# Kernel optimization log

Hardware: AMD Instinct MI355X
Metric: run time of the kernel (lower is better)

The kernel has to match this reference:

```python
import jax, jax.numpy as jnp
import numpy as np

ALPHA = 0.2

def _ema_last_weights(T, alpha, dtype):
    # Closed form for the final EMA value after the sequential recurrence:
    # ema_T = (1-a)^(T-1) * x_0 + sum_{t=1}^{T-1} a*(1-a)^(T-1-t) * x_t
    t = jnp.arange(T)
    w = alpha * (1.0 - alpha) ** (T - 1 - t)
    w = w.at[0].set((1.0 - alpha) ** (T - 1))
    return w.astype(dtype)


def setup_inputs() -> dict:
    key = jax.random.key(0)
    k1, k2 = jax.random.split(key)
    B, T, F = 64, 2048, 256
    x = jax.random.normal(k1, (B, T, F), dtype=jnp.float32)
    W = jax.random.normal(k2, (F, F), dtype=jnp.float32) * (1.0 / np.sqrt(F))
    b = jnp.zeros((F,), dtype=jnp.float32)
    return {"x": x, "W": W, "b": b}


def reference(x, W, b):
    B, T, F = x.shape
    # final-step EMA over time (equivalent to the sequential python loop)
    w = _ema_last_weights(T, ALPHA, x.dtype)          # [T]
    last_ref = jnp.einsum('t,btf->bf', w, x)[:, None, :]  # [B,1,F]
    # base residual predictor: per-timestep linear
    res = jnp.einsum('btf,fg->btg', x, W) + b          # [B,T,F]
    return last_ref + res
```

## Files before the change

### kernel.cpp

```cpp
#include <hip/hip_runtime.h>

#define Bdim 64
#define Tdim 2048
#define Fdim 256
#define TAIL 256
#define NCH 8
#define CHT 32

#define BK 32
#define NCHUNK 8
#define PFD 2

typedef __bf16 bf16x8 __attribute__((ext_vector_type(8)));
typedef float f32x16 __attribute__((ext_vector_type(16)));
typedef unsigned short u16x8 __attribute__((ext_vector_type(8)));

__device__ __forceinline__ unsigned short bf16_rne(float f) {
  unsigned int u = __float_as_uint(f);
  u += 0x7FFFu + ((u >> 16) & 1u);
  return (unsigned short)(u >> 16);
}

__global__ void prep(const float* __restrict__ x, const float* __restrict__ W,
                     unsigned short* __restrict__ Wf, float* __restrict__ part) {
  int blk = blockIdx.x;
  if (blk < Fdim) {
    int o = blk * 256 + threadIdx.x;
    int e = o & 7, lane = (o >> 3) & 63, nsub = (o >> 9) & 7, s = (o >> 12) & 1;
    int c = o >> 13;
    int n = nsub * 32 + (lane & 31);
    int k = c * 32 + (2 * s + (lane >> 5)) * 8 + e;
    Wf[o] = bf16_rne(W[k * Fdim + n]);
  } else {
    int j = blk - Fdim;
    int b = j & 63, c = j >> 6;
    int f = threadIdx.x;
    int t0 = Tdim - TAIL + c * CHT;
    float w = 0.2f * exp2f((float)(Tdim - 1 - t0) * -0.32192809488736235f);
    const float* xp = x + ((size_t)b * Tdim + t0) * Fdim + f;
    float s = 0.f;
#pragma unroll
    for (int q = 0; q < CHT; ++q) {
      s += w * xp[(size_t)q * Fdim];
      w *= 1.25f;
    }
    part[(c * Bdim + b) * Fdim + f] = s;
  }
}

__global__ __launch_bounds__(256, 3)
void gemm_fused(const float* __restrict__ x, const unsigned short* __restrict__ Wf,
                const float* __restrict__ bias, const float* __restrict__ part,
                float* __restrict__ out) {
  __shared__ float lref[Fdim];

  const int tid = threadIdx.x;
  const int blk = blockIdx.x;
  const int b = blk >> 5;
  const size_t row0 = (size_t)blk * 64;

  const int wave = tid >> 6;
  const int mw = wave >> 1;
  const int nw = wave & 1;
  const int lane = tid & 63;
  const int lm = lane & 31;
  const int half = lane >> 5;

  {
    float s = bias[tid];
#pragma unroll
    for (int c = 0; c < NCH; ++c) s += part[(c * Bdim + b) * Fdim + tid];
    lref[tid] = s;
  }
  __syncthreads();

  const float* ax = x + (row0 + mw * 32 + lm) * Fdim;
  const unsigned short* bx = Wf + (size_t)(nw * 4) * 512 + lane * 8;

  f32x16 acc[4] = {};
  float4 Ar[PFD][2][2];
  bf16x8 Bf[2][4];

#pragma unroll
  for (int p = 0; p < PFD; ++p) {
#pragma unroll
    for (int s = 0; s < 2; ++s) {
      const float* sp = ax + p * BK + (2 * s + half) * 8;
      Ar[p][s][0] = *(const float4*)sp;
      Ar[p][s][1] = *(const float4*)(sp + 4);
    }
  }
#pragma unroll
  for (int s = 0; s < 2; ++s)
#pragma unroll
    for (int j = 0; j < 4; ++j)
      Bf[s][j] = *(const bf16x8*)(bx + (size_t)(s * 8 + j) * 512);

#pragma unroll
  for (int c = 0; c < NCHUNK; ++c) {
    const int slot = c % PFD;
#pragma unroll
    for (int s = 0; s < 2; ++s) {
      float4 v0 = Ar[slot][s][0], v1 = Ar[slot][s][1];
      u16x8 w;
      w[0] = bf16_rne(v0.x); w[1] = bf16_rne(v0.y);
      w[2] = bf16_rne(v0.z); w[3] = bf16_rne(v0.w);
      w[4] = bf16_rne(v1.x); w[5] = bf16_rne(v1.y);
      w[6] = bf16_rne(v1.z); w[7] = bf16_rne(v1.w);
      bf16x8 af;
      *(u16x8*)&af = w;
      acc[0] = __builtin_amdgcn_mfma_f32_32x32x16_bf16(af, Bf[s][0], acc[0], 0, 0, 0);
      acc[1] = __builtin_amdgcn_mfma_f32_32x32x16_bf16(af, Bf[s][1], acc[1], 0, 0, 0);
      acc[2] = __builtin_amdgcn_mfma_f32_32x32x16_bf16(af, Bf[s][2], acc[2], 0, 0, 0);
      acc[3] = __builtin_amdgcn_mfma_f32_32x32x16_bf16(af, Bf[s][3], acc[3], 0, 0, 0);
      if (c + 1 < NCHUNK) {
#pragma unroll
        for (int j = 0; j < 4; ++j)
          Bf[s][j] = *(const bf16x8*)(bx + (size_t)(((c + 1) * 2 + s) * 8 + j) * 512);
      }
    }
    if (c + PFD < NCHUNK) {
#pragma unroll
      for (int s = 0; s < 2; ++s) {
        const float* sp = ax + (c + PFD) * BK + (2 * s + half) * 8;
        Ar[slot][s][0] = *(const float4*)sp;
        Ar[slot][s][1] = *(const float4*)(sp + 4);
      }
    }
  }

  float* op = out + (row0 + mw * 32) * Fdim + nw * 128;
  const int rbase = 4 * half;
#pragma unroll
  for (int j = 0; j < 4; ++j) {
    float lb = lref[nw * 128 + j * 32 + lm];
#pragma unroll
    for (int r = 0; r < 16; ++r) {
      int rowi = (r & 3) + 8 * (r >> 2) + rbase;
      op[(size_t)rowi * Fdim + j * 32 + lm] = acc[j][r] + lb;
    }
  }
}

extern "C" void kernel_launch(void* const* d_in, const int* in_sizes, int n_in,
                              void* d_out, int out_size, void* d_ws, size_t ws_size,
                              hipStream_t stream) {
  const float* x = (const float*)d_in[0];
  const float* W = (const float*)d_in[1];
  const float* bias = (const float*)d_in[2];
  float* out = (float*)d_out;

  unsigned short* Wf = (unsigned short*)d_ws;
  float* part = (float*)((char*)d_ws + Fdim * Fdim * sizeof(unsigned short));

  prep<<<Fdim + Bdim * NCH, 256, 0, stream>>>(x, W, Wf, part);
  gemm_fused<<<(Bdim * Tdim) / 64, 256, 0, stream>>>(x, Wf, bias, part, out);
}
```

Baseline: 285.7 us.

## Stage bf16 A fragments in LDS and retile waves to 64x64 output tiles

Before, each wave loaded and converted its own 32-row A slice straight from global memory, so two waves redundantly converted the same rows. Now all threads cooperatively load the 64x256 fp32 A tile once, convert it to bf16, and write it into a padded, XOR-swizzled LDS fragment layout. Each wave then computes a 64x64 output tile (2x2 MFMA blocks) with A fragments read from LDS, and the W fragment layout is reordered to match. The trade-offs are about 33KB of LDS per block, which may reduce occupancy, and an up-front sync, since global loads of A are no longer overlapped with the MFMAs.

```diff
diff --git a/kernel.cpp b/kernel.cpp
--- a/kernel.cpp
+++ b/kernel.cpp
@@ -7,9 +7,8 @@
 #define NCH 8
 #define CHT 32
 
-#define BK 32
 #define NCHUNK 8
-#define PFD 2
+#define FR_STR 520
 
 typedef __bf16 bf16x8 __attribute__((ext_vector_type(8)));
 typedef float f32x16 __attribute__((ext_vector_type(16)));
@@ -26,9 +25,9 @@
   int blk = blockIdx.x;
   if (blk < Fdim) {
     int o = blk * 256 + threadIdx.x;
-    int e = o & 7, lane = (o >> 3) & 63, nsub = (o >> 9) & 7, s = (o >> 12) & 1;
-    int c = o >> 13;
-    int n = nsub * 32 + (lane & 31);
+    int e = o & 7, lane = (o >> 3) & 63, wh = (o >> 9) & 1, s = (o >> 10) & 1;
+    int c = (o >> 11) & 7, w = o >> 14;
+    int n = w * 64 + wh * 32 + (lane & 31);
     int k = c * 32 + (2 * s + (lane >> 5)) * 8 + e;
     Wf[o] = bf16_rne(W[k * Fdim + n]);
   } else {
@@ -52,6 +51,7 @@
 void gemm_fused(const float* __restrict__ x, const unsigned short* __restrict__ Wf,
                 const float* __restrict__ bias, const float* __restrict__ part,
                 float* __restrict__ out) {
+  __shared__ unsigned short Afrag[32 * FR_STR];
   __shared__ float lref[Fdim];
 
   const int tid = threadIdx.x;
@@ -60,11 +60,23 @@
   const size_t row0 = (size_t)blk * 64;
 
   const int wave = tid >> 6;
-  const int mw = wave >> 1;
-  const int nw = wave & 1;
   const int lane = tid & 63;
   const int lm = lane & 31;
   const int half = lane >> 5;
+
+  const int r = tid >> 2, q = tid & 3;
+  const int iw = r >> 5;
+  const int sq = q >> 1, hb = q & 1;
+  const int dl = hb * 32 + (r & 31);
+  const int wpos = dl ^ ((dl >> 5) << 2);
+  const float* ap = x + (row0 + r) * Fdim + q * 8;
+
+  float4 av[8][2];
+#pragma unroll
+  for (int p = 0; p < 8; ++p) {
+    av[p][0] = *(const float4*)(ap + p * 32);
+    av[p][1] = *(const float4*)(ap + p * 32 + 4);
+  }
 
   {
     float s = bias[tid];
@@ -72,72 +84,70 @@
     for (int c = 0; c < NCH; ++c) s += part[(c * Bdim + b) * Fdim + tid];
     lref[tid] = s;
   }
+
+#pragma unroll
+  for (int p = 0; p < 8; ++p) {
+    float4 v0 = av[p][0], v1 = av[p][1];
+    u16x8 w;
+    w[0] = bf16_rne(v0.x); w[1] = bf16_rne(v0.y);
+    w[2] = bf16_rne(v0.z); w[3] = bf16_rne(v0.w);
+    w[4] = bf16_rne(v1.x); w[5] = bf16_rne(v1.y);
+    w[6] = bf16_rne(v1.z); w[7] = bf16_rne(v1.w);
+    const int fragidx = (p * 2 + iw) * 2 + sq;
+    *(u16x8*)&Afrag[fragidx * FR_STR + wpos * 8] = w;
+  }
   __syncthreads();
 
-  const float* ax = x + (row0 + mw * 32 + lm) * Fdim;
-  const unsigned short* bx = Wf + (size_t)(nw * 4) * 512 + lane * 8;
+  const unsigned short* bx = Wf + (size_t)wave * (32 * 512) + lane * 8;
+  const int rpos = lane ^ ((lane >> 5) << 2);
+  const unsigned short* abase = &Afrag[rpos * 8];
 
-  f32x16 acc[4] = {};
-  float4 Ar[PFD][2][2];
-  bf16x8 Bf[2][4];
+  f32x16 acc[2][2] = {};
+  bf16x8 Bf[2][2][2];
 
 #pragma unroll
-  for (int p = 0; p < PFD; ++p) {
+  for (int cc = 0; cc < 2; ++cc)
 #pragma unroll
-    for (int s = 0; s < 2; ++s) {
-      const float* sp = ax + p * BK + (2 * s + half) * 8;
-      Ar[p][s][0] = *(const float4*)sp;
-      Ar[p][s][1] = *(const float4*)(sp + 4);
-    }
-  }
+    for (int s = 0; s < 2; ++s)
 #pragma unroll
-  for (int s = 0; s < 2; ++s)
-#pragma unroll
-    for (int j = 0; j < 4; ++j)
-      Bf[s][j] = *(const bf16x8*)(bx + (size_t)(s * 8 + j) * 512);
+      for (int wh = 0; wh < 2; ++wh)
+        Bf[cc][s][wh] = *(const bf16x8*)(bx + (size_t)(cc * 4 + s * 2 + wh) * 512);
 
 #pragma unroll
   for (int c = 0; c < NCHUNK; ++c) {
-    const int slot = c % PFD;
+    const int par = c & 1;
 #pragma unroll
     for (int s = 0; s < 2; ++s) {
-      float4 v0 = Ar[slot][s][0], v1 = Ar[slot][s][1];
-      u16x8 w;
-      w[0] = bf16_rne(v0.x); w[1] = bf16_rne(v0.y);
-      w[2] = bf16_rne(v0.z); w[3] = bf16_rne(v0.w);
-      w[4] = bf16_rne(v1.x); w[5] = bf16_rne(v1.y);
-      w[6] = bf16_rne(v1.z); w[7] = bf16_rne(v1.w);
-      bf16x8 af;
-      *(u16x8*)&af = w;
-      acc[0] = __builtin_amdgcn_mfma_f32_32x32x16_bf16(af, Bf[s][0], acc[0], 0, 0, 0);
-      acc[1] = __builtin_amdgcn_mfma_f32_32x32x16_bf16(af, Bf[s][1], acc[1], 0, 0, 0);
-      acc[2] = __builtin_amdgcn_mfma_f32_32x32x16_bf16(af, Bf[s][2], acc[2], 0, 0, 0);
-      acc[3] = __builtin_amdgcn_mfma_f32_32x32x16_bf16(af, Bf[s][3], acc[3], 0, 0, 0);
-      if (c + 1 < NCHUNK) {
+      bf16x8 a0 = *(const bf16x8*)&abase[((c * 2 + 0) * 2 + s) * FR_STR];
+      bf16x8 a1 = *(const bf16x8*)&abase[((c * 2 + 1) * 2 + s) * FR_STR];
+      acc[0][0] = __builtin_amdgcn_mfma_f32_32x32x16_bf16(a0, Bf[par][s][0], acc[0][0], 0, 0, 0);
+      acc[0][1] = __builtin_amdgcn_mfma_f32_32x32x16_bf16(a0, Bf[par][s][1], acc[0][1], 0, 0, 0);
+      acc[1][0] = __builtin_amdgcn_mfma_f32_32x32x16_bf16(a1, Bf[par][s][0], acc[1][0], 0, 0, 0);
+      acc[1][1] = __builtin_amdgcn_mfma_f32_32x32x16_bf16(a1, Bf[par][s][1], acc[1][1], 0, 0, 0);
+    }
+    if (c + 2 < NCHUNK) {
 #pragma unroll
-        for (int j = 0; j < 4; ++j)
-          Bf[s][j] = *(const bf16x8*)(bx + (size_t)(((c + 1) * 2 + s) * 8 + j) * 512);
-      }
-    }
-    if (c + PFD < NCHUNK) {
+      for (int s = 0; s < 2; ++s)
 #pragma unroll
-      for (int s = 0; s < 2; ++s) {
-        const float* sp = ax + (c + PFD) * BK + (2 * s + half) * 8;
-        Ar[slot][s][0] = *(const float4*)sp;
-        Ar[slot][s][1] = *(const float4*)(sp + 4);
-      }
+        for (int wh = 0; wh < 2; ++wh)
+          Bf[par][s][wh] =
+              *(const bf16x8*)(bx + (size_t)((c + 2) * 4 + s * 2 + wh) * 512);
     }
   }
 
-  float* op = out + (row0 + mw * 32) * Fdim + nw * 128;
+  float* op = out + row0 * Fdim;
   const int rbase = 4 * half;
 #pragma unroll
-  for (int j = 0; j < 4; ++j) {
-    float lb = lref[nw * 128 + j * 32 + lm];
+  for (int i = 0; i < 2; ++i) {
 #pragma unroll
-    for (int r = 0; r < 16; ++r) {
-      int rowi = (r & 3) + 8 * (r >> 2) + rbase;
-      op[(size_t)rowi * Fdim + j * 32 + lm] = acc[j][r] + lb;
+    for (int j = 0; j < 2; ++j) {
+      int n = wave * 64 + j * 32 + lm;
+      float lb = lref[n];
+#pragma unroll
+      for (int rr = 0; rr < 16; ++rr) {
+        int rowi = i * 32 + (rr & 3) + 8 * (rr >> 2) + rbase;
+        op[(size_t)rowi * Fdim + n] = acc[i][j][rr] + lb;
+      }
     }
   }
 }
```

Result: faster. 243.1 us (-14.9%).

## Stage A tiles through per-wave LDS for coalesced row loads, reorder W fragments

Applied to the files above, without the earlier changes.

Changes the A-operand loading so each lane reads a 32-float contiguous row segment (eight lanes covering a row's 128-byte span). The values are converted to bf16 and written into a per-wave double-buffered LDS tile, then read back in MFMA fragment layout. The W fragment layout in prep is reordered so each wave's B reads are contiguous. The bias-plus-EMA reference is now kept per thread in registers, which removes the shared array and the __syncthreads. This trades strided global reads for an extra LDS round trip and more LDS usage, which may affect occupancy.

```diff
diff --git a/kernel.cpp b/kernel.cpp
--- a/kernel.cpp
+++ b/kernel.cpp
@@ -7,12 +7,11 @@
 #define NCH 8
 #define CHT 32
 
-#define BK 32
 #define NCHUNK 8
-#define PFD 2
 
 typedef __bf16 bf16x8 __attribute__((ext_vector_type(8)));
 typedef float f32x16 __attribute__((ext_vector_type(16)));
+typedef unsigned short u16x4 __attribute__((ext_vector_type(4)));
 typedef unsigned short u16x8 __attribute__((ext_vector_type(8)));
 
 __device__ __forceinline__ unsigned short bf16_rne(float f) {
@@ -23,18 +22,19 @@
 
 __global__ void prep(const float* __restrict__ x, const float* __restrict__ W,
                      unsigned short* __restrict__ Wf, float* __restrict__ part) {
-  int blk = blockIdx.x;
+  const int blk = blockIdx.x;
+  const int tid = threadIdx.x;
   if (blk < Fdim) {
-    int o = blk * 256 + threadIdx.x;
-    int e = o & 7, lane = (o >> 3) & 63, nsub = (o >> 9) & 7, s = (o >> 12) & 1;
-    int c = o >> 13;
-    int n = nsub * 32 + (lane & 31);
+    int o = blk * 256 + tid;
+    int e = o & 7, lane = (o >> 3) & 63, wh = (o >> 9) & 1, s = (o >> 10) & 1;
+    int c = (o >> 11) & 7, w = o >> 14;
+    int n = w * 64 + wh * 32 + (lane & 31);
     int k = c * 32 + (2 * s + (lane >> 5)) * 8 + e;
     Wf[o] = bf16_rne(W[k * Fdim + n]);
   } else {
     int j = blk - Fdim;
     int b = j & 63, c = j >> 6;
-    int f = threadIdx.x;
+    int f = tid;
     int t0 = Tdim - TAIL + c * CHT;
     float w = 0.2f * exp2f((float)(Tdim - 1 - t0) * -0.32192809488736235f);
     const float* xp = x + ((size_t)b * Tdim + t0) * Fdim + f;
@@ -52,88 +52,103 @@
 void gemm_fused(const float* __restrict__ x, const unsigned short* __restrict__ Wf,
                 const float* __restrict__ bias, const float* __restrict__ part,
                 float* __restrict__ out) {
-  __shared__ float lref[Fdim];
+  __shared__ unsigned short At[4][2][2][520];
 
   const int tid = threadIdx.x;
   const int blk = blockIdx.x;
   const int b = blk >> 5;
-  const size_t row0 = (size_t)blk * 64;
-
   const int wave = tid >> 6;
   const int mw = wave >> 1;
   const int nw = wave & 1;
   const int lane = tid & 63;
   const int lm = lane & 31;
   const int half = lane >> 5;
+  const size_t mt = (size_t)blk * 2 + mw;
 
-  {
-    float s = bias[tid];
+  float lref[4];
 #pragma unroll
-    for (int c = 0; c < NCH; ++c) s += part[(c * Bdim + b) * Fdim + tid];
-    lref[tid] = s;
+  for (int j = 0; j < 4; ++j) {
+    int n = nw * 128 + j * 32 + lm;
+    float s = bias[n];
+#pragma unroll
+    for (int c = 0; c < NCH; ++c) s += part[(c * Bdim + b) * Fdim + n];
+    lref[j] = s;
   }
-  __syncthreads();
 
-  const float* ax = x + (row0 + mw * 32 + lm) * Fdim;
-  const unsigned short* bx = Wf + (size_t)(nw * 4) * 512 + lane * 8;
+  const int arow = lane >> 3;
+  const int acol = (lane & 7) * 4;
+  const float* ax = x + (mt * 32 + arow) * Fdim + acol;
+  const int ds_ = ((lane & 7) >> 2);
+  const int dhb = ((lane & 7) >> 1) & 1;
+  const int dh2 = lane & 1;
+
+  const unsigned short* bx = Wf + lane * 8;
+#define BOFF(c, s, sub) \
+  ((size_t)(((nw * 2 + ((sub) >> 1)) * 32 + (c) * 4 + (s) * 2 + ((sub) & 1))) * 512)
 
   f32x16 acc[4] = {};
-  float4 Ar[PFD][2][2];
+  float4 Ar[2][4];
   bf16x8 Bf[2][4];
 
-#pragma unroll
-  for (int p = 0; p < PFD; ++p) {
-#pragma unroll
-    for (int s = 0; s < 2; ++s) {
-      const float* sp = ax + p * BK + (2 * s + half) * 8;
-      Ar[p][s][0] = *(const float4*)sp;
-      Ar[p][s][1] = *(const float4*)(sp + 4);
-    }
+#define ALOAD(k, slot)                                             \
+  {                                                                \
+    const float* s4 = ax + (k) * 32;                               \
+    Ar[slot][0] = *(const float4*)(s4);                            \
+    Ar[slot][1] = *(const float4*)(s4 + 8 * Fdim);                 \
+    Ar[slot][2] = *(const float4*)(s4 + 16 * Fdim);                \
+    Ar[slot][3] = *(const float4*)(s4 + 24 * Fdim);                \
   }
+#define ACVT(slot, buf)                                            \
+  {                                                                \
+    _Pragma("unroll") for (int p = 0; p < 4; ++p) {                \
+      float4 v = Ar[slot][p];                                      \
+      u16x4 wv;                                                    \
+      wv[0] = bf16_rne(v.x); wv[1] = bf16_rne(v.y);                \
+      wv[2] = bf16_rne(v.z); wv[3] = bf16_rne(v.w);                \
+      int dl = dhb * 32 + p * 8 + arow;                            \
+      *(u16x4*)&At[wave][buf][ds_][dl * 8 + dh2 * 4] = wv;         \
+    }                                                              \
+  }
+
+  ALOAD(0, 0);
+  ALOAD(1, 1);
 #pragma unroll
   for (int s = 0; s < 2; ++s)
 #pragma unroll
-    for (int j = 0; j < 4; ++j)
-      Bf[s][j] = *(const bf16x8*)(bx + (size_t)(s * 8 + j) * 512);
+    for (int sub = 0; sub < 4; ++sub)
+      Bf[s][sub] = *(const bf16x8*)(bx + BOFF(0, s, sub));
+  ACVT(0, 0);
 
 #pragma unroll
   for (int c = 0; c < NCHUNK; ++c) {
-    const int slot = c % PFD;
+    const int cur = c & 1, nxt = cur ^ 1;
+    if (c + 2 < NCHUNK) ALOAD(c + 2, cur);
+    bf16x8 a0 = *(const bf16x8*)&At[wave][cur][0][lane * 8];
+    bf16x8 a1 = *(const bf16x8*)&At[wave][cur][1][lane * 8];
+    if (c + 1 < NCHUNK) ACVT(nxt, nxt);
 #pragma unroll
     for (int s = 0; s < 2; ++s) {
-      float4 v0 = Ar[slot][s][0], v1 = Ar[slot][s][1];
-      u16x8 w;
-      w[0] = bf16_rne(v0.x); w[1] = bf16_rne(v0.y);
-      w[2] = bf16_rne(v0.z); w[3] = bf16_rne(v0.w);
-      w[4] = bf16_rne(v1.x); w[5] = bf16_rne(v1.y);
-      w[6] = bf16_rne(v1.z); w[7] = bf16_rne(v1.w);
-      bf16x8 af;
-      *(u16x8*)&af = w;
-      acc[0] = __builtin_amdgcn_mfma_f32_32x32x16_bf16(af, Bf[s][0], acc[0], 0, 0, 0);
-      acc[1] = __builtin_amdgcn_mfma_f32_32x32x16_bf16(af, Bf[s][1], acc[1], 0, 0, 0);
-      acc[2] = __builtin_amdgcn_mfma_f32_32x32x16_bf16(af, Bf[s][2], acc[2], 0, 0, 0);
-      acc[3] = __builtin_amdgcn_mfma_f32_32x32x16_bf16(af, Bf[s][3], acc[3], 0, 0, 0);
+      bf16x8 a = (s == 0) ? a0 : a1;
+      acc[0] = __builtin_amdgcn_mfma_f32_32x32x16_bf16(a, Bf[s][0], acc[0], 0, 0, 0);
+      acc[1] = __builtin_amdgcn_mfma_f32_32x32x16_bf16(a, Bf[s][1], acc[1], 0, 0, 0);
+      acc[2] = __builtin_amdgcn_mfma_f32_32x32x16_bf16(a, Bf[s][2], acc[2], 0, 0, 0);
+      acc[3] = __builtin_amdgcn_mfma_f32_32x32x16_bf16(a, Bf[s][3], acc[3], 0, 0, 0);
       if (c + 1 < NCHUNK) {
 #pragma unroll
-        for (int j = 0; j < 4; ++j)
-          Bf[s][j] = *(const bf16x8*)(bx + (size_t)(((c + 1) * 2 + s) * 8 + j) * 512);
-      }
-    }
-    if (c + PFD < NCHUNK) {
-#pragma unroll
-      for (int s = 0; s < 2; ++s) {
-        const float* sp = ax + (c + PFD) * BK + (2 * s + half) * 8;
-        Ar[slot][s][0] = *(const float4*)sp;
-        Ar[slot][s][1] = *(const float4*)(sp + 4);
+        for (int sub = 0; sub < 4; ++sub)
+          Bf[s][sub] = *(const bf16x8*)(bx + BOFF(c + 1, s, sub));
       }
     }
   }
+#undef BOFF
+#undef ALOAD
+#undef ACVT
 
-  float* op = out + (row0 + mw * 32) * Fdim + nw * 128;
+  float* op = out + mt * 32 * Fdim + nw * 128;
   const int rbase = 4 * half;
 #pragma unroll
   for (int j = 0; j < 4; ++j) {
-    float lb = lref[nw * 128 + j * 32 + lm];
+    float lb = lref[j];
 #pragma unroll
     for (int r = 0; r < 16; ++r) {
       int rowi = (r & 3) + 8 * (r >> 2) + rbase;
@@ -151,7 +166,7 @@
   float* out = (float*)d_out;
 
   unsigned short* Wf = (unsigned short*)d_ws;
-  float* part = (float*)((char*)d_ws + Fdim * Fdim * sizeof(unsigned short));
+  float* part = (float*)((char*)d_ws + 131072);
 
   prep<<<Fdim + Bdim * NCH, 256, 0, stream>>>(x, W, Wf, part);
   gemm_fused<<<(Bdim * Tdim) / 64, 256, 0, stream>>>(x, Wf, bias, part, out);
```

Measured after the change: 256.8 us. 10.1% less time.

## Stage A tiles via global_load_lds with 16x16 MFMA and 32-row blocks

Applied to the files above, without the earlier changes.

Replaces direct per-lane register loads of the fp32 x tile with asynchronous global_load_lds into a 4-deep swizzled LDS ring buffer, synchronised with vmcnt waits and barriers. Switches from 32x32x16 to 16x16x32 bf16 MFMA, with each wave owning 64 output columns of a 32-row block. The W fragment layout in prep changes to match. The grid doubles and the occupancy hint rises to 5, aiming to hide memory latency. The risk is that W fragments are now re-read by twice as many blocks, and the extra barriers add sync overhead.

```diff
diff --git a/kernel.cpp b/kernel.cpp
--- a/kernel.cpp
+++ b/kernel.cpp
@@ -7,13 +7,10 @@
 #define NCH 8
 #define CHT 32
 
-#define BK 32
 #define NCHUNK 8
-#define PFD 2
 
 typedef __bf16 bf16x8 __attribute__((ext_vector_type(8)));
-typedef float f32x16 __attribute__((ext_vector_type(16)));
-typedef unsigned short u16x8 __attribute__((ext_vector_type(8)));
+typedef float f32x4 __attribute__((ext_vector_type(4)));
 
 __device__ __forceinline__ unsigned short bf16_rne(float f) {
   unsigned int u = __float_as_uint(f);
@@ -21,20 +18,26 @@
   return (unsigned short)(u >> 16);
 }
 
+__device__ __forceinline__ void gll16(const float* g, float* l) {
+  __builtin_amdgcn_global_load_lds(
+      (const __attribute__((address_space(1))) void*)g,
+      (__attribute__((address_space(3))) void*)l, 16, 0, 0);
+}
+
 __global__ void prep(const float* __restrict__ x, const float* __restrict__ W,
                      unsigned short* __restrict__ Wf, float* __restrict__ part) {
-  int blk = blockIdx.x;
+  const int blk = blockIdx.x;
+  const int tid = threadIdx.x;
   if (blk < Fdim) {
-    int o = blk * 256 + threadIdx.x;
-    int e = o & 7, lane = (o >> 3) & 63, nsub = (o >> 9) & 7, s = (o >> 12) & 1;
-    int c = o >> 13;
-    int n = nsub * 32 + (lane & 31);
-    int k = c * 32 + (2 * s + (lane >> 5)) * 8 + e;
+    int o = blk * 256 + tid;
+    int e = o & 7, lane = (o >> 3) & 63, nt = (o >> 9) & 15, c = o >> 13;
+    int n = nt * 16 + (lane & 15);
+    int k = c * 32 + (lane >> 4) * 8 + e;
     Wf[o] = bf16_rne(W[k * Fdim + n]);
   } else {
     int j = blk - Fdim;
     int b = j & 63, c = j >> 6;
-    int f = threadIdx.x;
+    int f = tid;
     int t0 = Tdim - TAIL + c * CHT;
     float w = 0.2f * exp2f((float)(Tdim - 1 - t0) * -0.32192809488736235f);
     const float* xp = x + ((size_t)b * Tdim + t0) * Fdim + f;
@@ -48,23 +51,22 @@
   }
 }
 
-__global__ __launch_bounds__(256, 3)
+__global__ __launch_bounds__(256, 5)
 void gemm_fused(const float* __restrict__ x, const unsigned short* __restrict__ Wf,
                 const float* __restrict__ bias, const float* __restrict__ part,
                 float* __restrict__ out) {
+  __shared__ float Abuf[4][32 * 32];
   __shared__ float lref[Fdim];
 
   const int tid = threadIdx.x;
   const int blk = blockIdx.x;
-  const int b = blk >> 5;
-  const size_t row0 = (size_t)blk * 64;
-
-  const int wave = tid >> 6;
-  const int mw = wave >> 1;
-  const int nw = wave & 1;
+  const int b = blk >> 6;
+  const size_t row0 = (size_t)blk * 32;
+  const int w = tid >> 6;
   const int lane = tid & 63;
-  const int lm = lane & 31;
-  const int half = lane >> 5;
+  const int l15 = lane & 15;
+  const int g = lane >> 4;
+  const int q0 = (2 * g) ^ (lane & 7);
 
   {
     float s = bias[tid];
@@ -74,70 +76,71 @@
   }
   __syncthreads();
 
-  const float* ax = x + (row0 + mw * 32 + lm) * Fdim;
-  const unsigned short* bx = Wf + (size_t)(nw * 4) * 512 + lane * 8;
+  const int srow = (lane >> 3);
+  const float* gsrc =
+      x + (row0 + w * 8 + srow) * Fdim + (((lane & 7) ^ srow) << 2);
+  const unsigned short* bx = Wf + (size_t)(w * 4) * 512 + lane * 8;
 
-  f32x16 acc[4] = {};
-  float4 Ar[PFD][2][2];
+  f32x4 acc[2][4] = {};
   bf16x8 Bf[2][4];
 
+  gll16(gsrc + 0 * 32, &Abuf[0][w * 256]);
+  gll16(gsrc + 1 * 32, &Abuf[1][w * 256]);
+  gll16(gsrc + 2 * 32, &Abuf[2][w * 256]);
 #pragma unroll
-  for (int p = 0; p < PFD; ++p) {
-#pragma unroll
-    for (int s = 0; s < 2; ++s) {
-      const float* sp = ax + p * BK + (2 * s + half) * 8;
-      Ar[p][s][0] = *(const float4*)sp;
-      Ar[p][s][1] = *(const float4*)(sp + 4);
-    }
-  }
-#pragma unroll
-  for (int s = 0; s < 2; ++s)
-#pragma unroll
-    for (int j = 0; j < 4; ++j)
-      Bf[s][j] = *(const bf16x8*)(bx + (size_t)(s * 8 + j) * 512);
+  for (int ntl = 0; ntl < 4; ++ntl)
+    Bf[0][ntl] = *(const bf16x8*)(bx + (size_t)(0 * 16 + ntl) * 512);
+  asm volatile("s_waitcnt vmcnt(6)" ::: "memory");
+  __builtin_amdgcn_s_barrier();
 
 #pragma unroll
   for (int c = 0; c < NCHUNK; ++c) {
-    const int slot = c % PFD;
+    if (c + 1 < NCHUNK) {
 #pragma unroll
-    for (int s = 0; s < 2; ++s) {
-      float4 v0 = Ar[slot][s][0], v1 = Ar[slot][s][1];
-      u16x8 w;
-      w[0] = bf16_rne(v0.x); w[1] = bf16_rne(v0.y);
-      w[2] = bf16_rne(v0.z); w[3] = bf16_rne(v0.w);
-      w[4] = bf16_rne(v1.x); w[5] = bf16_rne(v1.y);
-      w[6] = bf16_rne(v1.z); w[7] = bf16_rne(v1.w);
+      for (int ntl = 0; ntl < 4; ++ntl)
+        Bf[(c + 1) & 1][ntl] =
+            *(const bf16x8*)(bx + (size_t)((c + 1) * 16 + ntl) * 512);
+    }
+    if (c + 3 < NCHUNK)
+      gll16(gsrc + (c + 3) * 32, &Abuf[(c + 3) & 3][w * 256]);
+
+    bf16x8 a[2];
+#pragma unroll
+    for (int m = 0; m < 2; ++m) {
+      const float* lp = &Abuf[c & 3][(m * 16 + l15) * 32];
+      f32x4 lo = *(const f32x4*)(lp + q0 * 4);
+      f32x4 hi = *(const f32x4*)(lp + (q0 ^ 1) * 4);
       bf16x8 af;
-      *(u16x8*)&af = w;
-      acc[0] = __builtin_amdgcn_mfma_f32_32x32x16_bf16(af, Bf[s][0], acc[0], 0, 0, 0);
-      acc[1] = __builtin_amdgcn_mfma_f32_32x32x16_bf16(af, Bf[s][1], acc[1], 0, 0, 0);
-      acc[2] = __builtin_amdgcn_mfma_f32_32x32x16_bf16(af, Bf[s][2], acc[2], 0, 0, 0);
-      acc[3] = __builtin_amdgcn_mfma_f32_32x32x16_bf16(af, Bf[s][3], acc[3], 0, 0, 0);
-      if (c + 1 < NCHUNK) {
+      af[0] = (__bf16)lo[0]; af[1] = (__bf16)lo[1];
+      af[2] = (__bf16)lo[2]; af[3] = (__bf16)lo[3];
+      af[4] = (__bf16)hi[0]; af[5] = (__bf16)hi[1];
+      af[6] = (__bf16)hi[2]; af[7] = (__bf16)hi[3];
+      a[m] = af;
+    }
 #pragma unroll
-        for (int j = 0; j < 4; ++j)
-          Bf[s][j] = *(const bf16x8*)(bx + (size_t)(((c + 1) * 2 + s) * 8 + j) * 512);
-      }
-    }
-    if (c + PFD < NCHUNK) {
+    for (int m = 0; m < 2; ++m)
 #pragma unroll
-      for (int s = 0; s < 2; ++s) {
-        const float* sp = ax + (c + PFD) * BK + (2 * s + half) * 8;
-        Ar[slot][s][0] = *(const float4*)sp;
-        Ar[slot][s][1] = *(const float4*)(sp + 4);
-      }
+      for (int ntl = 0; ntl < 4; ++ntl)
+        acc[m][ntl] = __builtin_amdgcn_mfma_f32_16x16x32_bf16(
+            a[m], Bf[c & 1][ntl], acc[m][ntl], 0, 0, 0);
+
+    if (c + 1 < NCHUNK) {
+      asm volatile("s_waitcnt vmcnt(8)" ::: "memory");
+      __builtin_amdgcn_s_barrier();
     }
   }
 
-  float* op = out + (row0 + mw * 32) * Fdim + nw * 128;
-  const int rbase = 4 * half;
+  float* op = out + row0 * Fdim;
+  const int r4 = g * 4;
 #pragma unroll
-  for (int j = 0; j < 4; ++j) {
-    float lb = lref[nw * 128 + j * 32 + lm];
+  for (int m = 0; m < 2; ++m) {
 #pragma unroll
-    for (int r = 0; r < 16; ++r) {
-      int rowi = (r & 3) + 8 * (r >> 2) + rbase;
-      op[(size_t)rowi * Fdim + j * 32 + lm] = acc[j][r] + lb;
+    for (int ntl = 0; ntl < 4; ++ntl) {
+      const int col = w * 64 + ntl * 16 + l15;
+      const float lb = lref[col];
+#pragma unroll
+      for (int r = 0; r < 4; ++r)
+        op[(size_t)(m * 16 + r4 + r) * Fdim + col] = acc[m][ntl][r] + lb;
     }
   }
 }
@@ -151,8 +154,8 @@
   float* out = (float*)d_out;
 
   unsigned short* Wf = (unsigned short*)d_ws;
-  float* part = (float*)((char*)d_ws + Fdim * Fdim * sizeof(unsigned short));
+  float* part = (float*)((char*)d_ws + 131072);
 
   prep<<<Fdim + Bdim * NCH, 256, 0, stream>>>(x, W, Wf, part);
-  gemm_fused<<<(Bdim * Tdim) / 64, 256, 0, stream>>>(x, Wf, bias, part, out);
+  gemm_fused<<<(Bdim * Tdim) / 32, 256, 0, stream>>>(x, Wf, bias, part, out);
 }
```

Measured after the change: 258.5 us. 1.11x faster.
